# Kernel tuning notes

Hardware: AMD Instinct MI355X
Metric: run time of the kernel (lower is better)

The kernel has to match this reference:

```python
import jax, jax.numpy as jnp
import numpy as np

D = 768
HEAD_SIZE = 64  # D // 12


def setup_inputs() -> dict:
    key = jax.random.key(0)
    k_ix, k_wk, k_wq, k_wv = jax.random.split(key, 4)
    ix = jax.random.normal(k_ix, (4, 4096, D), dtype=jnp.float32)
    s = 1.0 / np.sqrt(D)
    Wk = jax.random.normal(k_wk, (D, HEAD_SIZE), dtype=jnp.float32) * s
    Wq = jax.random.normal(k_wq, (D, HEAD_SIZE), dtype=jnp.float32) * s
    Wv = jax.random.normal(k_wv, (D, HEAD_SIZE), dtype=jnp.float32) * s
    return {"ix": ix, "Wk": Wk, "Wq": Wq, "Wv": Wv}


def reference(ix, Wk, Wq, Wv):
    # ix: [B, N, D]; W*: [D, h]
    k = ix @ Wk            # [B, N, h]
    q = ix @ Wq            # [B, N, h]
    v = ix @ Wv            # [B, N, h]
    scale = HEAD_SIZE ** -0.5
    wei = jnp.einsum('bnh,bmh->bnm', q, k) * scale  # [B, N, N]
    wei = jax.nn.softmax(wei, axis=-1)
    out = jnp.einsum('bnm,bmh->bnh', wei, v)        # [B, N, h]
    return out
```

## Files before the change

kernel.cpp:

```cpp
#include <hip/hip_runtime.h>
#include <math.h>

#define Dm   768
#define Hm   64
#define SEQ  4096
#define NB   4
#define NROW (NB * SEQ)

#define QSCALE (0.125f * 1.4426950408889634f)

typedef _Float16 f16;
typedef __attribute__((ext_vector_type(8))) _Float16 f16x8;
typedef __attribute__((ext_vector_type(2))) __fp16 fp16x2_raw;
typedef __attribute__((ext_vector_type(4))) float f32x4;
typedef unsigned int uint;
typedef unsigned short ushort;

#define MFMAH(A, B, C) __builtin_amdgcn_mfma_f32_16x16x32_f16(A, B, C, 0, 0, 0)

__device__ __forceinline__ uint pkrtz(float a, float b) {
    fp16x2_raw r = __builtin_amdgcn_cvt_pkrtz(a, b);
    return __builtin_bit_cast(uint, r);
}
__device__ __forceinline__ ushort f2h(float f) {
    f16 h = (f16)f;
    return __builtin_bit_cast(ushort, h);
}
union F16x8U { uint u[4]; f16x8 v; };

__global__ __launch_bounds__(256) void wconv(
    const float* __restrict__ Wq, const float* __restrict__ Wk,
    const float* __restrict__ Wv, ushort* __restrict__ WTt)
{
    __shared__ ushort lt[64 * 33];
    const int b  = blockIdx.x;
    const int kt = b / 3, m = b - kt * 3;
    const float* W = (m == 0) ? Wq : (m == 1 ? Wk : Wv);
    const float sc = (m == 0) ? QSCALE : 1.0f;
    const int t = threadIdx.x;
#pragma unroll
    for (int p = 0; p < 8; ++p) {
        int t2 = p * 256 + t;
        int kl = t2 >> 6, c = t2 & 63;
        lt[c * 33 + kl] = f2h(W[(size_t)(kt * 32 + kl) * 64 + c] * sc);
    }
    __syncthreads();
#pragma unroll
    for (int p = 0; p < 8; ++p) {
        int t2 = p * 256 + t;
        int c = t2 >> 5, kk = t2 & 31;
        WTt[((size_t)kt * 192 + m * 64 + c) * 32 + kk] = lt[c * 33 + kk];
    }
}

__global__ __launch_bounds__(256, 2) void proj(
    const float* __restrict__ ix, const ushort* __restrict__ WTt,
    ushort* __restrict__ Qw, ushort* __restrict__ Kt, ushort* __restrict__ Vt)
{
    __shared__ __align__(16) float comb[2][2][3072];

    const int t    = threadIdx.x;
    const int lane = t & 63;
    const int kh   = __builtin_amdgcn_readfirstlane(t >> 6);
    const int q15  = lane & 15, quad = lane >> 4;
    const int gr0  = blockIdx.x * 32;

    const float* Ab0 = ix + (size_t)(gr0 + q15) * Dm + kh * 192 + quad * 8;
    const float* Ab1 = Ab0 + (size_t)16 * Dm;
    const ushort* Bb = WTt + ((size_t)(kh * 6) * 192 + q15) * 32 + quad * 8;

    f32x4 acc[2][12];
#pragma unroll
    for (int rt = 0; rt < 2; ++rt)
#pragma unroll
        for (int ct = 0; ct < 12; ++ct) acc[rt][ct] = (f32x4){0.f, 0.f, 0.f, 0.f};

    f32x4 Af[2][3][2];
#pragma unroll
    for (int i = 0; i < 2; ++i) {
        Af[0][i][0] = *(const f32x4*)(Ab0 + i * 32);
        Af[0][i][1] = *(const f32x4*)(Ab0 + i * 32 + 4);
        Af[1][i][0] = *(const f32x4*)(Ab1 + i * 32);
        Af[1][i][1] = *(const f32x4*)(Ab1 + i * 32 + 4);
    }

#pragma unroll
    for (int it = 0; it < 6; ++it) {
        f16x8 Bf[12];
#pragma unroll
        for (int ct = 0; ct < 12; ++ct)
            Bf[ct] = *(const f16x8*)(Bb + (size_t)it * 6144 + ct * 512);

        if (it + 2 < 6) {
            Af[0][(it + 2) % 3][0] = *(const f32x4*)(Ab0 + (it + 2) * 32);
            Af[0][(it + 2) % 3][1] = *(const f32x4*)(Ab0 + (it + 2) * 32 + 4);
            Af[1][(it + 2) % 3][0] = *(const f32x4*)(Ab1 + (it + 2) * 32);
            Af[1][(it + 2) % 3][1] = *(const f32x4*)(Ab1 + (it + 2) * 32 + 4);
        }

        F16x8U af0, af1;
        af0.u[0] = pkrtz(Af[0][it % 3][0].x, Af[0][it % 3][0].y);
        af0.u[1] = pkrtz(Af[0][it % 3][0].z, Af[0][it % 3][0].w);
        af0.u[2] = pkrtz(Af[0][it % 3][1].x, Af[0][it % 3][1].y);
        af0.u[3] = pkrtz(Af[0][it % 3][1].z, Af[0][it % 3][1].w);
        af1.u[0] = pkrtz(Af[1][it % 3][0].x, Af[1][it % 3][0].y);
        af1.u[1] = pkrtz(Af[1][it % 3][0].z, Af[1][it % 3][0].w);
        af1.u[2] = pkrtz(Af[1][it % 3][1].x, Af[1][it % 3][1].y);
        af1.u[3] = pkrtz(Af[1][it % 3][1].z, Af[1][it % 3][1].w);
        __builtin_amdgcn_s_setprio(1);
#pragma unroll
        for (int ct = 0; ct < 12; ++ct) {
            acc[0][ct] = MFMAH(af0.v, Bf[ct], acc[0][ct]);
            acc[1][ct] = MFMAH(af1.v, Bf[ct], acc[1][ct]);
        }
        __builtin_amdgcn_s_setprio(0);
    }

    if (kh >= 2) {
#pragma unroll
        for (int rt = 0; rt < 2; ++rt)
#pragma unroll
            for (int ct = 0; ct < 12; ++ct)
                *(f32x4*)&comb[rt][kh - 2][(ct * 64 + lane) * 4] = acc[rt][ct];
    }
    __syncthreads();
    if (kh < 2) {
#pragma unroll
        for (int rt = 0; rt < 2; ++rt)
#pragma unroll
            for (int ct = 0; ct < 12; ++ct) {
                f32x4 o = *(const f32x4*)&comb[rt][kh][(ct * 64 + lane) * 4];
                acc[rt][ct].x += o.x; acc[rt][ct].y += o.y;
                acc[rt][ct].z += o.z; acc[rt][ct].w += o.w;
            }
    }
    __syncthreads();
    if (kh == 1) {
#pragma unroll
        for (int rt = 0; rt < 2; ++rt)
#pragma unroll
            for (int ct = 0; ct < 12; ++ct)
                *(f32x4*)&comb[rt][0][(ct * 64 + lane) * 4] = acc[rt][ct];
    }
    __syncthreads();
    if (kh == 0) {
#pragma unroll
        for (int rt = 0; rt < 2; ++rt) {
#pragma unroll
            for (int ct = 0; ct < 12; ++ct) {
                f32x4 o = *(const f32x4*)&comb[rt][0][(ct * 64 + lane) * 4];
                acc[rt][ct].x += o.x; acc[rt][ct].y += o.y;
                acc[rt][ct].z += o.z; acc[rt][ct].w += o.w;
            }
            const int gr  = gr0 + rt * 16;
            const int n4  = gr >> 4;
            const int h16 = n4 & 1;
            const int j32 = gr >> 5;
#pragma unroll
            for (int ct = 0; ct < 12; ++ct) {
                float vals[4] = {acc[rt][ct].x, acc[rt][ct].y, acc[rt][ct].z, acc[rt][ct].w};
                if (ct < 4) {
#pragma unroll
                    for (int r = 0; r < 4; ++r)
                        Qw[(size_t)(gr + quad * 4 + r) * 64 + ct * 16 + q15] = f2h(vals[r]);
                } else if (ct < 8) {
#pragma unroll
                    for (int r = 0; r < 4; ++r)
                        Kt[(size_t)n4 * 1024 + (ct - 4) * 256 + (quad * 4 + r) * 16 + q15] = f2h(vals[r]);
                } else {
                    ushort4 vv;
                    vv.x = f2h(vals[0]); vv.y = f2h(vals[1]);
                    vv.z = f2h(vals[2]); vv.w = f2h(vals[3]);
                    *(ushort4*)(Vt + (size_t)j32 * 2048 + (ct - 8) * 512 +
                                (h16 * 2 + (quad >> 1)) * 128 + q15 * 8 + (quad & 1) * 4) = vv;
                }
            }
        }
    }
}

#define OSTR 68
#define OBUF 4352

__global__ __launch_bounds__(512, 2) void attn(
    const ushort* __restrict__ Qw, const ushort* __restrict__ Kt,
    const ushort* __restrict__ Vt, float* __restrict__ out)
{
    __shared__ __align__(16) float aF[20992];
    short* aS = (short*)aF;

    const int t    = threadIdx.x;
    const int lane = t & 63;
    const int w    = __builtin_amdgcn_readfirstlane(t >> 6);
    const int q15  = lane & 15, quad = lane >> 4;

    const int bb    = blockIdx.x;
    const int xcd   = bb & 7;
    const int batch = xcd >> 1;
    const int slot  = (bb >> 3) | ((xcd & 1) << 5);
    const int q0    = slot * 64;
    const size_t base = (size_t)batch * SEQ;

    f16x8 qf[4][2];
#pragma unroll
    for (int g = 0; g < 4; ++g)
#pragma unroll
        for (int h = 0; h < 2; ++h)
            qf[g][h] = *(const f16x8*)(Qw + (base + q0 + g * 16 + q15) * 64 + h * 32 + quad * 8);

    f32x4 oacc[4][4];
#pragma unroll
    for (int g = 0; g < 4; ++g)
#pragma unroll
        for (int dt = 0; dt < 4; ++dt) oacc[g][dt] = (f32x4){0.f, 0.f, 0.f, 0.f};
    float lsum[4] = {0.f, 0.f, 0.f, 0.f};

    const size_t j0g = base + w * 512;
    const ushort* Kfb = Kt + (j0g >> 4) * 1024;
    const ushort* Vfb = Vt + (j0g >> 5) * 2048 + lane * 8;
    short* Ps = aS + w * 5120;

    int koff[2][2];
#pragma unroll
    for (int jt = 0; jt < 2; ++jt)
#pragma unroll
        for (int h = 0; h < 2; ++h)
            koff[jt][h] = jt * 1024 + h * 512 + (quad >> 1) * 256 + q15 * 16 + (quad & 1) * 8;

    f16x8 kf[2][2][2], vf[2][4];
    f32x4 zz[4][2];
    f16x8 pf[4];

#define LOADKV(slotc, i)                                                       \
    {                                                                          \
        _Pragma("unroll") for (int jt = 0; jt < 2; ++jt)                       \
        _Pragma("unroll") for (int h = 0; h < 2; ++h)                          \
            kf[slotc][jt][h] = *(const f16x8*)(Kfb + (size_t)(i) * 2048 + koff[jt][h]); \
        _Pragma("unroll") for (int dt = 0; dt < 4; ++dt)                       \
            vf[slotc][dt] = *(const f16x8*)(Vfb + (size_t)(i) * 2048 + dt * 512); \
    }
#define QKMM(slotc)                                                            \
    {                                                                          \
        _Pragma("unroll") for (int g = 0; g < 4; ++g)                          \
        _Pragma("unroll") for (int jt = 0; jt < 2; ++jt) {                     \
            f32x4 z = (f32x4){0.f, 0.f, 0.f, 0.f};                             \
            z = MFMAH(kf[slotc][jt][0], qf[g][0], z);                          \
            z = MFMAH(kf[slotc][jt][1], qf[g][1], z);                          \
            zz[g][jt] = z;                                                     \
        }                                                                      \
    }
#define SMPACK(pb)                                                             \
    {                                                                          \
        _Pragma("unroll") for (int g = 0; g < 4; ++g)                          \
        _Pragma("unroll") for (int jt = 0; jt < 2; ++jt) {                     \
            float e0 = exp2f(zz[g][jt].x), e1 = exp2f(zz[g][jt].y);            \
            float e2 = exp2f(zz[g][jt].z), e3 = exp2f(zz[g][jt].w);            \
            lsum[g] += (e0 + e1) + (e2 + e3);                                  \
            uint2 pk = make_uint2(pkrtz(e0, e1), pkrtz(e2, e3));               \
            *(uint2*)(Ps + (pb) * 2560 + (g * 16 + q15) * 40 + jt * 16 + quad * 4) = pk; \
        }                                                                      \
    }
#define PFLOAD(pb)                                                             \
    {                                                                          \
        _Pragma("unroll") for (int g = 0; g < 4; ++g)                          \
            pf[g] = *(const f16x8*)(Ps + (pb) * 2560 + (g * 16 + q15) * 40 + quad * 8); \
    }
#define PVMM(slotc)                                                            \
    {                                                                          \
        _Pragma("unroll") for (int dt = 0; dt < 4; ++dt)                       \
        _Pragma("unroll") for (int g = 0; g < 4; ++g)                          \
            oacc[g][dt] = MFMAH(pf[g], vf[slotc][dt], oacc[g][dt]);            \
    }

    LOADKV(0, 0);
    LOADKV(1, 1);
    QKMM(0);
    SMPACK(0);
#pragma unroll
    for (int i = 0; i < 16; ++i) {
        PFLOAD(i & 1);
        __builtin_amdgcn_s_setprio(1);
        if (i + 1 < 16) QKMM((i + 1) & 1);
        PVMM(i & 1);
        __builtin_amdgcn_s_setprio(0);
        if (i + 2 < 16) LOADKV(i & 1, i + 2);
        if (i + 1 < 16) SMPACK((i + 1) & 1);
    }

#pragma unroll
    for (int g = 0; g < 4; ++g) {
        lsum[g] += __shfl_xor(lsum[g], 16);
        lsum[g] += __shfl_xor(lsum[g], 32);
    }
    if (quad == 0) {
#pragma unroll
        for (int g = 0; g < 4; ++g)
            aF[20480 + w * 64 + g * 16 + q15] = lsum[g];
    }
    __syncthreads();

#define OWRITE(idx)                                                          \
    {                                                                        \
        float* b = aF + (idx) * OBUF;                                        \
        _Pragma("unroll") for (int g = 0; g < 4; ++g)                        \
        _Pragma("unroll") for (int dt = 0; dt < 4; ++dt) {                   \
            b[(g * 16 + quad * 4 + 0) * OSTR + dt * 16 + q15] = oacc[g][dt].x; \
            b[(g * 16 + quad * 4 + 1) * OSTR + dt * 16 + q15] = oacc[g][dt].y; \
            b[(g * 16 + quad * 4 + 2) * OSTR + dt * 16 + q15] = oacc[g][dt].z; \
            b[(g * 16 + quad * 4 + 3) * OSTR + dt * 16 + q15] = oacc[g][dt].w; \
        }                                                                    \
    }
#define OADD(idx)                                                            \
    {                                                                        \
        const float* b = aF + (idx) * OBUF;                                  \
        _Pragma("unroll") for (int g = 0; g < 4; ++g)                        \
        _Pragma("unroll") for (int dt = 0; dt < 4; ++dt) {                   \
            oacc[g][dt].x += b[(g * 16 + quad * 4 + 0) * OSTR + dt * 16 + q15];\
            oacc[g][dt].y += b[(g * 16 + quad * 4 + 1) * OSTR + dt * 16 + q15];\
            oacc[g][dt].z += b[(g * 16 + quad * 4 + 2) * OSTR + dt * 16 + q15];\
            oacc[g][dt].w += b[(g * 16 + quad * 4 + 3) * OSTR + dt * 16 + q15];\
        }                                                                    \
    }
    if (w >= 4) OWRITE(w - 4);
    __syncthreads();
    if (w < 4) OADD(w);
    __syncthreads();
    if (w == 2 || w == 3) OWRITE(w - 2);
    __syncthreads();
    if (w < 2) OADD(w);
    __syncthreads();
    if (w < 2) OWRITE(w);
    __syncthreads();

    {
        const int q  = t >> 3;
        const int d0 = (t & 7) * 8;
        float l = 0.f;
#pragma unroll
        for (int i = 0; i < 8; ++i) l += aF[20480 + i * 64 + q];
        const float linv = 1.0f / l;
#pragma unroll
        for (int k2 = 0; k2 < 2; ++k2) {
            float4 a = *(const float4*)&aF[q * OSTR + d0 + k2 * 4];
            float4 b = *(const float4*)&aF[OBUF + q * OSTR + d0 + k2 * 4];
            float4 s;
            s.x = (a.x + b.x) * linv; s.y = (a.y + b.y) * linv;
            s.z = (a.z + b.z) * linv; s.w = (a.w + b.w) * linv;
            *(float4*)(out + (base + q0 + q) * 64 + d0 + k2 * 4) = s;
        }
    }
}

extern "C" void kernel_launch(void* const* d_in, const int* in_sizes, int n_in,
                              void* d_out, int out_size, void* d_ws, size_t ws_size,
                              hipStream_t stream)
{
    const float* ix = (const float*)d_in[0];
    const float* Wk = (const float*)d_in[1];
    const float* Wq = (const float*)d_in[2];
    const float* Wv = (const float*)d_in[3];
    float* out = (float*)d_out;

    ushort* Qw  = (ushort*)d_ws;
    ushort* Kt  = Qw + (size_t)NROW * Hm;
    ushort* Vt  = Kt + (size_t)NROW * Hm;
    ushort* WTt = Vt + (size_t)NROW * Hm;

    wconv<<<72, 256, 0, stream>>>(Wq, Wk, Wv, WTt);
    proj<<<512, 256, 0, stream>>>(ix, WTt, Qw, Kt, Vt);
    attn<<<256, 512, 0, stream>>>(Qw, Kt, Vt, out);
}
```

Baseline: 128.0 us.

## Split attention KV range across two blocks and combine partials in new kernel

Each query tile's 4096 keys are now split into two halves handled by separate blocks, which doubles the grid to 512 blocks. Each wave processes 256 keys instead of 512, and the block writes unnormalized partial outputs and row sums to workspace. A new fincomb kernel adds the two halves and normalizes. LDS padding is shrunk and launch bounds raised so more blocks fit per CU. The cost is extra global traffic for the partials, an additional kernel launch, and a longer serial reduction chain inside the block.

```diff
diff --git a/kernel.cpp b/kernel.cpp
--- a/kernel.cpp
+++ b/kernel.cpp
@@ -179,14 +179,19 @@
     }
 }
 
+#define PSTR 36
+#define PWAVE 4608
+#define PBUF 2304
 #define OSTR 68
 #define OBUF 4352
-
-__global__ __launch_bounds__(512, 2) void attn(
+#define LOFF 18432
+
+__global__ __launch_bounds__(512, 4) void attn(
     const ushort* __restrict__ Qw, const ushort* __restrict__ Kt,
-    const ushort* __restrict__ Vt, float* __restrict__ out)
+    const ushort* __restrict__ Vt, float* __restrict__ oP,
+    float* __restrict__ lP)
 {
-    __shared__ __align__(16) float aF[20992];
+    __shared__ __align__(16) float aF[18944];
     short* aS = (short*)aF;
 
     const int t    = threadIdx.x;
@@ -197,7 +202,8 @@
     const int bb    = blockIdx.x;
     const int xcd   = bb & 7;
     const int batch = xcd >> 1;
-    const int slot  = (bb >> 3) | ((xcd & 1) << 5);
+    const int jh    = xcd & 1;
+    const int slot  = bb >> 3;
     const int q0    = slot * 64;
     const size_t base = (size_t)batch * SEQ;
 
@@ -215,10 +221,10 @@
         for (int dt = 0; dt < 4; ++dt) oacc[g][dt] = (f32x4){0.f, 0.f, 0.f, 0.f};
     float lsum[4] = {0.f, 0.f, 0.f, 0.f};
 
-    const size_t j0g = base + w * 512;
+    const size_t j0g = base + jh * 2048 + w * 256;
     const ushort* Kfb = Kt + (j0g >> 4) * 1024;
     const ushort* Vfb = Vt + (j0g >> 5) * 2048 + lane * 8;
-    short* Ps = aS + w * 5120;
+    short* Ps = aS + w * PWAVE;
 
     int koff[2][2];
 #pragma unroll
@@ -257,13 +263,13 @@
             float e2 = exp2f(zz[g][jt].z), e3 = exp2f(zz[g][jt].w);            \
             lsum[g] += (e0 + e1) + (e2 + e3);                                  \
             uint2 pk = make_uint2(pkrtz(e0, e1), pkrtz(e2, e3));               \
-            *(uint2*)(Ps + (pb) * 2560 + (g * 16 + q15) * 40 + jt * 16 + quad * 4) = pk; \
+            *(uint2*)(Ps + (pb) * PBUF + (g * 16 + q15) * PSTR + jt * 16 + quad * 4) = pk; \
         }                                                                      \
     }
 #define PFLOAD(pb)                                                             \
     {                                                                          \
         _Pragma("unroll") for (int g = 0; g < 4; ++g)                          \
-            pf[g] = *(const f16x8*)(Ps + (pb) * 2560 + (g * 16 + q15) * 40 + quad * 8); \
+            pf[g] = *(const f16x8*)(Ps + (pb) * PBUF + (g * 16 + q15) * PSTR + quad * 8); \
     }
 #define PVMM(slotc)                                                            \
     {                                                                          \
@@ -277,14 +283,14 @@
     QKMM(0);
     SMPACK(0);
 #pragma unroll
-    for (int i = 0; i < 16; ++i) {
+    for (int i = 0; i < 8; ++i) {
         PFLOAD(i & 1);
         __builtin_amdgcn_s_setprio(1);
-        if (i + 1 < 16) QKMM((i + 1) & 1);
+        if (i + 1 < 8) QKMM((i + 1) & 1);
         PVMM(i & 1);
         __builtin_amdgcn_s_setprio(0);
-        if (i + 2 < 16) LOADKV(i & 1, i + 2);
-        if (i + 1 < 16) SMPACK((i + 1) & 1);
+        if (i + 2 < 8) LOADKV(i & 1, i + 2);
+        if (i + 1 < 8) SMPACK((i + 1) & 1);
     }
 
 #pragma unroll
@@ -295,7 +301,7 @@
     if (quad == 0) {
 #pragma unroll
         for (int g = 0; g < 4; ++g)
-            aF[20480 + w * 64 + g * 16 + q15] = lsum[g];
+            aF[LOFF + w * 64 + g * 16 + q15] = lsum[g];
     }
     __syncthreads();
 
@@ -321,34 +327,61 @@
             oacc[g][dt].w += b[(g * 16 + quad * 4 + 3) * OSTR + dt * 16 + q15];\
         }                                                                    \
     }
-    if (w >= 4) OWRITE(w - 4);
-    __syncthreads();
-    if (w < 4) OADD(w);
-    __syncthreads();
-    if (w == 2 || w == 3) OWRITE(w - 2);
-    __syncthreads();
-    if (w < 2) OADD(w);
-    __syncthreads();
-    if (w < 2) OWRITE(w);
+    if (w == 4) OWRITE(0);
+    if (w == 5) OWRITE(1);
+    __syncthreads();
+    if (w == 0) OADD(0);
+    if (w == 1) OADD(1);
+    __syncthreads();
+    if (w == 6) OWRITE(0);
+    if (w == 7) OWRITE(1);
+    __syncthreads();
+    if (w == 2) OADD(0);
+    if (w == 3) OADD(1);
+    __syncthreads();
+    if (w == 2) OWRITE(0);
+    if (w == 3) OWRITE(1);
+    __syncthreads();
+    if (w == 0) OADD(0);
+    if (w == 1) OADD(1);
+    __syncthreads();
+    if (w == 1) OWRITE(0);
+    __syncthreads();
+    if (w == 0) OADD(0);
+    __syncthreads();
+    if (w == 0) OWRITE(0);
     __syncthreads();
 
     {
         const int q  = t >> 3;
         const int d0 = (t & 7) * 8;
-        float l = 0.f;
-#pragma unroll
-        for (int i = 0; i < 8; ++i) l += aF[20480 + i * 64 + q];
-        const float linv = 1.0f / l;
-#pragma unroll
-        for (int k2 = 0; k2 < 2; ++k2) {
-            float4 a = *(const float4*)&aF[q * OSTR + d0 + k2 * 4];
-            float4 b = *(const float4*)&aF[OBUF + q * OSTR + d0 + k2 * 4];
-            float4 s;
-            s.x = (a.x + b.x) * linv; s.y = (a.y + b.y) * linv;
-            s.z = (a.z + b.z) * linv; s.w = (a.w + b.w) * linv;
-            *(float4*)(out + (base + q0 + q) * 64 + d0 + k2 * 4) = s;
+        float* od = oP + ((size_t)jh * NROW + base + q0 + q) * 64 + d0;
+#pragma unroll
+        for (int k2 = 0; k2 < 2; ++k2)
+            *(float4*)(od + k2 * 4) = *(const float4*)&aF[q * OSTR + d0 + k2 * 4];
+        if (t < 64) {
+            float l = 0.f;
+#pragma unroll
+            for (int i = 0; i < 8; ++i) l += aF[LOFF + i * 64 + t];
+            lP[(size_t)jh * NROW + base + q0 + t] = l;
         }
     }
+}
+
+__global__ __launch_bounds__(256) void fincomb(
+    const float* __restrict__ oP, const float* __restrict__ lP,
+    float* __restrict__ out)
+{
+    const int i4  = blockIdx.x * 256 + threadIdx.x;
+    const int row = i4 >> 4;
+    const float l = lP[row] + lP[NROW + row];
+    const float r = 1.0f / l;
+    const float4 a = ((const float4*)oP)[i4];
+    const float4 b = ((const float4*)oP)[(size_t)NROW * 16 + i4];
+    float4 s;
+    s.x = (a.x + b.x) * r; s.y = (a.y + b.y) * r;
+    s.z = (a.z + b.z) * r; s.w = (a.w + b.w) * r;
+    ((float4*)out)[i4] = s;
 }
 
 extern "C" void kernel_launch(void* const* d_in, const int* in_sizes, int n_in,
@@ -365,8 +398,11 @@
     ushort* Kt  = Qw + (size_t)NROW * Hm;
     ushort* Vt  = Kt + (size_t)NROW * Hm;
     ushort* WTt = Vt + (size_t)NROW * Hm;
+    float*  oP  = (float*)(WTt + 147456);
+    float*  lP  = oP + (size_t)2 * NROW * Hm;
 
     wconv<<<72, 256, 0, stream>>>(Wq, Wk, Wv, WTt);
     proj<<<512, 256, 0, stream>>>(ix, WTt, Qw, Kt, Vt);
-    attn<<<256, 512, 0, stream>>>(Qw, Kt, Vt, out);
-}
+    attn<<<512, 512, 0, stream>>>(Qw, Kt, Vt, oP, lP);
+    fincomb<<<1024, 256, 0, stream>>>(oP, lP, out);
+}
```

Result: slower. 280.7 us (+119.4%).
